# Kernel tuning notes

Measured on AMD Instinct MI355X. Metric: run time of the kernel, lower is better.

The kernel has to match this reference:

```python
import jax, jax.numpy as jnp
import numpy as np

NUM_USERS = 100000
NUM_ITEMS = 50000
NUM_EDGES = 4000000
EMB_DIM = 64
K_HOPS = 3


def setup_inputs() -> dict:
    key = jax.random.key(0)
    k1, k2, k3, k4, k5, k6 = jax.random.split(key, 6)
    N = NUM_USERS + NUM_ITEMS
    return {
        "users_emb": jax.random.normal(k1, (NUM_USERS, EMB_DIM), dtype=jnp.float32) * 0.1,
        "items_emb": jax.random.normal(k2, (NUM_ITEMS, EMB_DIM), dtype=jnp.float32) * 0.1,
        "edge_row": jax.random.randint(k3, (NUM_EDGES,), 0, N, dtype=jnp.int32),
        "edge_col": jax.random.randint(k4, (NUM_EDGES,), 0, N, dtype=jnp.int32),
        "user_id": jax.random.randint(k5, (4096,), 0, NUM_USERS, dtype=jnp.int32),
        "item_ids": jax.random.randint(k6, (4096,), 0, NUM_ITEMS, dtype=jnp.int32),
    }


def reference(users_emb, items_emb, edge_row, edge_col, user_id, item_ids):
    num_users = users_emb.shape[0]
    N = num_users + items_emb.shape[0]
    dt = users_emb.dtype

    # gcn_norm (no self loops): deg = rowsum of A, w_e = d_r^{-1/2} d_c^{-1/2}
    deg = jax.ops.segment_sum(jnp.ones(edge_row.shape[0], dtype=dt), edge_row,
                              num_segments=N)
    deg_inv_sqrt = jnp.where(deg > 0, 1.0 / jnp.sqrt(jnp.where(deg > 0, deg, 1.0)), 0.0)
    w = deg_inv_sqrt[edge_row] * deg_inv_sqrt[edge_col]  # [E]

    emb = jnp.concatenate([users_emb, items_emb], axis=0)  # [N, D]
    acc = emb  # running sum of K+1 layer snapshots
    for _ in range(K_HOPS):
        # SpMM: out[r] += w_e * emb[c]
        emb = jax.ops.segment_sum(w[:, None] * emb[edge_col], edge_row,
                                  num_segments=N)
        acc = acc + emb
    emb_final = acc / (K_HOPS + 1)  # layer-mean pooling

    users_final = emb_final[user_id]               # [B, D]
    items_final = emb_final[num_users + item_ids]  # [B, D]
    return jnp.concatenate([users_final, items_final], axis=1)  # [B, 2D]
```

## Files before the change

kernel.cpp:

```cpp
#include <hip/hip_runtime.h>
#include <hip/hip_bf16.h>

#define NUSERS 100000
#define NITEMS 50000
#define NN (NUSERS + NITEMS)
#define NE 4000000
#define DIM 64
#define BQ 4096
#define NBIN ((NN + 255) >> 8)
#define BINCAP 9216
#define EPB2 8192

typedef unsigned short u16;
typedef unsigned int u32;
typedef float v2f __attribute__((ext_vector_type(2)));

__device__ __forceinline__ float bf2f(u16 u) {
    return __uint_as_float(((unsigned)u) << 16);
}
__device__ __forceinline__ u16 f2bf(float f) {
    unsigned x = __float_as_uint(f);
    return (u16)((x + 0x7FFFu + ((x >> 16) & 1u)) >> 16);
}
__device__ __forceinline__ void add8p(v2f* acc2, uint4 u) {
    acc2[0] += (v2f){__uint_as_float(u.x << 16), __uint_as_float(u.x & 0xffff0000u)};
    acc2[1] += (v2f){__uint_as_float(u.y << 16), __uint_as_float(u.y & 0xffff0000u)};
    acc2[2] += (v2f){__uint_as_float(u.z << 16), __uint_as_float(u.z & 0xffff0000u)};
    acc2[3] += (v2f){__uint_as_float(u.w << 16), __uint_as_float(u.w & 0xffff0000u)};
}
__device__ __forceinline__ uint4 ld_row(const char* __restrict__ base, int c, int dgoff) {
    u32 off = ((u32)c << 7) + (u32)dgoff;
    return *(const uint4*)(base + off);
}

__device__ __forceinline__ void rowsum_core(int start, int n8, int c_all,
                                            const int* __restrict__ col_s,
                                            const char* __restrict__ inb,
                                            int eslot, int dgoff, v2f* acc2) {
    int G = n8 >> 3;
    if (G <= 8) {
        int cg[8];
#pragma unroll
        for (int g = 0; g < 8; ++g)
            cg[g] = __shfl(c_all, (g << 3) + eslot, 64);
        uint4 v[8];
#pragma unroll
        for (int g = 0; g < 8; ++g)
            if (g < G) v[g] = ld_row(inb, cg[g], dgoff);
#pragma unroll
        for (int g = 0; g < 8; ++g)
            if (g < G) add8p(acc2, v[g]);
    } else {
        int i = eslot;
        int c0 = col_s[start + i];
        uint4 v0 = ld_row(inb, c0, dgoff);
        for (i += 8; i < n8; i += 8) {
            int c1 = col_s[start + i];
            uint4 v1 = ld_row(inb, c1, dgoff);
            add8p(acc2, v0);
            v0 = v1;
        }
        add8p(acc2, v0);
    }
}

__device__ __forceinline__ void reduce_acc(v2f* acc2) {
#pragma unroll
    for (int off = 8; off <= 32; off <<= 1)
#pragma unroll
        for (int j = 0; j < 4; ++j) {
            v2f o;
            o.x = __shfl_xor(acc2[j].x, off, 64);
            o.y = __shfl_xor(acc2[j].y, off, 64);
            acc2[j] += o;
        }
}

__global__ void k_init(int* __restrict__ bin_cur, u32* __restrict__ m2w,
                       u16* __restrict__ ea, u16* __restrict__ eb) {
    int t = blockIdx.x * blockDim.x + threadIdx.x;
    if (t < NBIN) bin_cur[t] = t * BINCAP;
    if (t < 37504) m2w[t] = 0;
    if (t < 32) {
        ((u32*)(ea + (size_t)NN * DIM))[t] = 0;
        ((u32*)(eb + (size_t)NN * DIM))[t] = 0;
    }
}

__global__ void __launch_bounds__(1024) k_binA2(
        const int* __restrict__ row, const int* __restrict__ col,
        int* __restrict__ bin_cur, u32* __restrict__ pairs, int E) {
    __shared__ u32 stage[EPB2];
    __shared__ int hist[NBIN];
    __shared__ int base_l[NBIN];
    __shared__ int cbase[NBIN];
    __shared__ int lcur[NBIN];
    __shared__ int s[1024];
    int t = threadIdx.x;
    int base = blockIdx.x * EPB2;
    int lim = min(E - base, EPB2);

    if (t < NBIN) hist[t] = 0;
    __syncthreads();

    for (int i = t; i < lim; i += 1024)
        atomicAdd(&hist[row[base + i] >> 8], 1);
    __syncthreads();

    int v = (t < NBIN) ? hist[t] : 0;
    s[t] = v;
    __syncthreads();
    for (int off = 1; off < 1024; off <<= 1) {
        int x = (t >= off) ? s[t - off] : 0;
        __syncthreads();
        s[t] += x;
        __syncthreads();
    }
    if (t < NBIN) {
        int excl = s[t] - v;
        base_l[t] = excl;
        lcur[t] = excl;
        cbase[t] = (v > 0) ? atomicAdd(&bin_cur[t], v) : 0;
    }
    __syncthreads();

    for (int i = t; i < lim; i += 1024) {
        int r = row[base + i];
        int c = col[base + i];
        int pos = atomicAdd(&lcur[r >> 8], 1);
        stage[pos] = ((u32)(r & 255) << 24) | (u32)c;
    }
    __syncthreads();

    int wv = t >> 6;
    int lane = t & 63;
    for (int b = wv; b < NBIN; b += 16) {
        int h = hist[b];
        int lb = base_l[b];
        size_t gb = (size_t)cbase[b];
        for (int i = lane; i < h; i += 64)
            pairs[gb + i] = stage[lb + i];
    }
}

__global__ void __launch_bounds__(1024) k_binB(
        const u32* __restrict__ pairs, const int* __restrict__ bin_cur,
        int* __restrict__ col_s, int* __restrict__ rs, int* __restrict__ deg) {
    __shared__ int cnt[256];
    __shared__ int pscan[256];
    __shared__ int cur[256];
    int b = blockIdx.x;
    int t = threadIdx.x;
    int base = b * BINCAP;
    int end = bin_cur[b];
    if (t < 256) cnt[t] = 0;
    __syncthreads();
    for (int i = base + t; i < end; i += 1024)
        atomicAdd(&cnt[pairs[i] >> 24], 1);
    __syncthreads();
    int v = (t < 256) ? cnt[t] : 0;
    int pv = (v + 7) & ~7;
    if (t < 256) pscan[t] = pv;
    __syncthreads();
    for (int off = 1; off < 256; off <<= 1) {
        int x = (t >= off && t < 256) ? pscan[t - off] : 0;
        __syncthreads();
        if (t < 256) pscan[t] += x;
        __syncthreads();
    }
    if (t < 256) {
        int rowstart = base + pscan[t] - pv;
        int r = (b << 8) + t;
        if (r < NN) {
            rs[r] = rowstart;
            deg[r] = v;
        }
        cur[t] = rowstart;
        for (int i = v; i < pv; ++i) col_s[rowstart + i] = NN;
    }
    __syncthreads();
    for (int i = base + t; i < end; i += 1024) {
        u32 p = pairs[i];
        int pos = atomicAdd(&cur[p >> 24], 1);
        col_s[pos] = (int)(p & 0x00FFFFFFu);
    }
}

__global__ void k_concat_t0(const float* __restrict__ u, const float* __restrict__ it,
                            const int* __restrict__ deg, u16* __restrict__ emb) {
    int i = blockIdx.x * blockDim.x + threadIdx.x;
    const int NU4 = NUSERS * DIM / 4;
    const int NT4 = NN * DIM / 4;
    if (i >= NT4) return;
    int row = i >> 4;
    int d = deg[row];
    float sc = (d > 0) ? (1.0f / sqrtf((float)d)) : 0.0f;
    float4 v = (i < NU4) ? ((const float4*)u)[i] : ((const float4*)it)[i - NU4];
    ushort4 o;
    o.x = f2bf(sc * v.x); o.y = f2bf(sc * v.y);
    o.z = f2bf(sc * v.z); o.w = f2bf(sc * v.w);
    ((ushort4*)emb)[i] = o;
}

__global__ void k_mark(const int* __restrict__ uid, const int* __restrict__ iid,
                       const int* __restrict__ rs, const int* __restrict__ deg,
                       const int* __restrict__ col_s, unsigned char* __restrict__ m2) {
    int q = (blockIdx.x * blockDim.x + threadIdx.x) >> 6;
    if (q >= 2 * BQ) return;
    int lane = threadIdx.x & 63;
    int r = (q < BQ) ? uid[q] : (NUSERS + iid[q - BQ]);
    if (lane == 0) m2[r] = 1;
    int s = rs[r], n = deg[r];
    for (int i = lane; i < n; i += 64) m2[col_s[s + i]] = 1;
}

__global__ void k_spmm8(const int* __restrict__ rs, const int* __restrict__ deg,
                        const int* __restrict__ col_s, const u16* __restrict__ in,
                        u16* __restrict__ out, const unsigned char* __restrict__ mask) {
    int wid = (blockIdx.x * blockDim.x + threadIdx.x) >> 6;
    if (wid >= NN) return;
    if (mask && !mask[wid]) return;
    int lane = threadIdx.x & 63;
    int eslot = lane >> 3;
    int dg = lane & 7;
    int dgoff = dg << 4;
    int n = deg[wid];
    int start = rs[wid];
    int n8 = (n + 7) & ~7;
    int c_all = col_s[start + lane];
    const char* inb = (const char*)in;
    v2f acc2[4] = {(v2f)0.f, (v2f)0.f, (v2f)0.f, (v2f)0.f};
    if (n8 > 0)
        rowsum_core(start, n8, c_all, col_s, inb, eslot, dgoff, acc2);
    reduce_acc(acc2);
    if (eslot == 0) {
        float s = (n > 0) ? (1.0f / (float)n) : 0.0f;
        v2f vs = {s, s};
        u32 p[4];
#pragma unroll
        for (int j = 0; j < 4; ++j) {
            v2f r = acc2[j] * vs;
            __hip_bfloat162 h = __float22bfloat162_rn(make_float2(r.x, r.y));
            p[j] = *(u32*)&h;
        }
        ((uint4*)out)[(size_t)wid * 8 + dg] = make_uint4(p[0], p[1], p[2], p[3]);
    }
}

__global__ void k_spmm_out(const int* __restrict__ rs, const int* __restrict__ deg,
                           const int* __restrict__ col_s, const u16* __restrict__ in,
                           const int* __restrict__ uid, const int* __restrict__ iid,
                           float* __restrict__ out) {
    int q = (blockIdx.x * blockDim.x + threadIdx.x) >> 6;
    if (q >= 2 * BQ) return;
    int lane = threadIdx.x & 63;
    int eslot = lane >> 3;
    int dg = lane & 7;
    int dgoff = dg << 4;
    int b, r, off;
    if (q < BQ) { b = q; r = uid[q]; off = 0; }
    else { b = q - BQ; r = NUSERS + iid[q - BQ]; off = DIM; }
    int n = deg[r];
    int start = rs[r];
    int n8 = (n + 7) & ~7;
    int c_all = col_s[start + lane];
    const char* inb = (const char*)in;
    v2f acc2[4] = {(v2f)0.f, (v2f)0.f, (v2f)0.f, (v2f)0.f};
    if (n8 > 0)
        rowsum_core(start, n8, c_all, col_s, inb, eslot, dgoff, acc2);
    reduce_acc(acc2);
    if (eslot == 0) {
        float dr = (n > 0) ? (1.0f / sqrtf((float)n)) : 0.0f;
        float* o = out + (size_t)b * (2 * DIM) + off + dg * 8;
#pragma unroll
        for (int j = 0; j < 4; ++j) {
            o[2 * j]     = (o[2 * j]     + dr * acc2[j].x) * 0.25f;
            o[2 * j + 1] = (o[2 * j + 1] + dr * acc2[j].y) * 0.25f;
        }
    }
}


__global__ void k_gather_init(const int* __restrict__ uid, const int* __restrict__ iid,
                              const float* __restrict__ u, const float* __restrict__ it,
                              float* __restrict__ out) {
    int t = blockIdx.x * blockDim.x + threadIdx.x;
    if (t >= BQ * DIM) return;
    int b = t >> 6;
    int d = t & 63;
    out[b * (2 * DIM) + d]       = u[(size_t)uid[b] * DIM + d];
    out[b * (2 * DIM) + DIM + d] = it[(size_t)iid[b] * DIM + d];
}

__global__ void k_gather_add(const int* __restrict__ uid, const int* __restrict__ iid,
                             const int* __restrict__ deg, const u16* __restrict__ emb,
                             float* __restrict__ out) {
    int t = blockIdx.x * blockDim.x + threadIdx.x;
    if (t >= BQ * DIM) return;
    int b = t >> 6;
    int d = t & 63;
    int ru = uid[b];
    int ri = NUSERS + iid[b];
    int du = deg[ru], di = deg[ri];
    float su = (du > 0) ? sqrtf((float)du) : 0.0f;
    float si = (di > 0) ? sqrtf((float)di) : 0.0f;
    int ou = b * (2 * DIM) + d;
    int oi = ou + DIM;
    out[ou] = out[ou] + su * bf2f(emb[(size_t)ru * DIM + d]);
    out[oi] = out[oi] + si * bf2f(emb[(size_t)ri * DIM + d]);
}


extern "C" void kernel_launch(void* const* d_in, const int* in_sizes, int n_in,
                              void* d_out, int out_size, void* d_ws, size_t ws_size,
                              hipStream_t stream) {
    const float* users_emb = (const float*)d_in[0];
    const float* items_emb = (const float*)d_in[1];
    const int*   edge_row  = (const int*)d_in[2];
    const int*   edge_col  = (const int*)d_in[3];
    const int*   user_id   = (const int*)d_in[4];
    const int*   item_ids  = (const int*)d_in[5];
    float* out = (float*)d_out;

    char* ws = (char*)d_ws;
    int*   deg_i   = (int*)  (ws + 0);
    int*   rs      = (int*)  (ws + 655360);
    int*   bin_cur = (int*)  (ws + 1310720);
    unsigned char* m2 = (unsigned char*)(ws + 1400000);
    int*   col_s   = (int*)  (ws + 4194304);
    u32*   pairs   = (u32*)  (ws + 29360128);
    u16*   emb_a   = (u16*)  (ws + 54525952);
    u16*   emb_b   = (u16*)  (ws + 75497472);

    k_init<<<147, 256, 0, stream>>>(bin_cur, (u32*)m2, emb_a, emb_b);

    k_binA2<<<(NE + EPB2 - 1) / EPB2, 1024, 0, stream>>>(edge_row, edge_col, bin_cur,
                                                         pairs, NE);
    k_binB<<<NBIN, 1024, 0, stream>>>(pairs, bin_cur, col_s, rs, deg_i);

    k_concat_t0<<<(NN * DIM / 4 + 255) / 256, 256, 0, stream>>>(users_emb, items_emb,
                                                                deg_i, emb_a);

    k_gather_init<<<(BQ * DIM + 255) / 256, 256, 0, stream>>>(user_id, item_ids,
                                                              users_emb, items_emb, out);

    k_mark<<<(2 * BQ + 3) / 4, 256, 0, stream>>>(user_id, item_ids, rs, deg_i, col_s, m2);

    const int spmm_blocks = (NN + 3) / 4;
    k_spmm8<<<spmm_blocks, 256, 0, stream>>>(rs, deg_i, col_s, emb_a, emb_b,
                                             (const unsigned char*)nullptr);
    k_gather_add<<<(BQ * DIM + 255) / 256, 256, 0, stream>>>(user_id, item_ids, deg_i,
                                                             emb_b, out);
    k_spmm8<<<spmm_blocks, 256, 0, stream>>>(rs, deg_i, col_s, emb_b, emb_a, m2);
    k_gather_add<<<(BQ * DIM + 255) / 256, 256, 0, stream>>>(user_id, item_ids, deg_i,
                                                             emb_a, out);
    k_spmm_out<<<(2 * BQ + 3) / 4, 256, 0, stream>>>(rs, deg_i, col_s, emb_a,
                                                     user_id, item_ids, out);
}
```

Baseline: 307.1 us.

## Fuse embedding scaling into binning, sort columns by range, fold gather_add into output

The binning kernel now sub-buckets each row's columns into coarse column ranges, so the CSR column lists come out roughly sorted and later gathers touch memory more locally. The separate concat/scale kernel is folded into the binning kernel, which removes one launch and one extra pass over the per-row degrees. The last gather_add is dropped and its contribution is added inside the output SpMM by reloading the query row. This costs more shared memory and atomics in k_binB and some extra work per query in the final kernel.

```diff
diff --git a/kernel.cpp b/kernel.cpp
--- a/kernel.cpp
+++ b/kernel.cpp
@@ -10,6 +10,8 @@
 #define NBIN ((NN + 255) >> 8)
 #define BINCAP 9216
 #define EPB2 8192
+#define PSH 14
+#define NP 10
 
 typedef unsigned short u16;
 typedef unsigned int u32;
@@ -145,20 +147,33 @@
 
 __global__ void __launch_bounds__(1024) k_binB(
         const u32* __restrict__ pairs, const int* __restrict__ bin_cur,
-        int* __restrict__ col_s, int* __restrict__ rs, int* __restrict__ deg) {
-    __shared__ int cnt[256];
+        int* __restrict__ col_s, int* __restrict__ rs, int* __restrict__ deg,
+        const float* __restrict__ uemb, const float* __restrict__ itemb,
+        u16* __restrict__ emb) {
+    __shared__ int cnt2[256 * NP];
+    __shared__ int cur2[256 * NP];
     __shared__ int pscan[256];
-    __shared__ int cur[256];
+    __shared__ int degl[256];
     int b = blockIdx.x;
     int t = threadIdx.x;
     int base = b * BINCAP;
     int end = bin_cur[b];
-    if (t < 256) cnt[t] = 0;
-    __syncthreads();
-    for (int i = base + t; i < end; i += 1024)
-        atomicAdd(&cnt[pairs[i] >> 24], 1);
-    __syncthreads();
-    int v = (t < 256) ? cnt[t] : 0;
+    for (int i = t; i < 256 * NP; i += 1024) cnt2[i] = 0;
+    __syncthreads();
+
+    for (int i = base + t; i < end; i += 1024) {
+        u32 p = pairs[i];
+        int row = p >> 24;
+        int c = (int)(p & 0x00FFFFFFu);
+        atomicAdd(&cnt2[row * NP + (c >> PSH)], 1);
+    }
+    __syncthreads();
+
+    int v = 0;
+    if (t < 256) {
+#pragma unroll
+        for (int q = 0; q < NP; ++q) v += cnt2[t * NP + q];
+    }
     int pv = (v + 7) & ~7;
     if (t < 256) pscan[t] = pv;
     __syncthreads();
@@ -170,36 +185,44 @@
     }
     if (t < 256) {
         int rowstart = base + pscan[t] - pv;
+        degl[t] = v;
         int r = (b << 8) + t;
         if (r < NN) {
             rs[r] = rowstart;
             deg[r] = v;
         }
-        cur[t] = rowstart;
+        int acc = rowstart;
+#pragma unroll
+        for (int q = 0; q < NP; ++q) {
+            cur2[t * NP + q] = acc;
+            acc += cnt2[t * NP + q];
+        }
         for (int i = v; i < pv; ++i) col_s[rowstart + i] = NN;
     }
     __syncthreads();
+
     for (int i = base + t; i < end; i += 1024) {
         u32 p = pairs[i];
-        int pos = atomicAdd(&cur[p >> 24], 1);
-        col_s[pos] = (int)(p & 0x00FFFFFFu);
-    }
-}
-
-__global__ void k_concat_t0(const float* __restrict__ u, const float* __restrict__ it,
-                            const int* __restrict__ deg, u16* __restrict__ emb) {
-    int i = blockIdx.x * blockDim.x + threadIdx.x;
-    const int NU4 = NUSERS * DIM / 4;
-    const int NT4 = NN * DIM / 4;
-    if (i >= NT4) return;
-    int row = i >> 4;
-    int d = deg[row];
-    float sc = (d > 0) ? (1.0f / sqrtf((float)d)) : 0.0f;
-    float4 v = (i < NU4) ? ((const float4*)u)[i] : ((const float4*)it)[i - NU4];
-    ushort4 o;
-    o.x = f2bf(sc * v.x); o.y = f2bf(sc * v.y);
-    o.z = f2bf(sc * v.z); o.w = f2bf(sc * v.w);
-    ((ushort4*)emb)[i] = o;
+        int row = p >> 24;
+        int c = (int)(p & 0x00FFFFFFu);
+        int pos = atomicAdd(&cur2[row * NP + (c >> PSH)], 1);
+        col_s[pos] = c;
+    }
+
+    int r0 = b << 8;
+    for (int sIdx = t; sIdx < 256 * 16; sIdx += 1024) {
+        int rl = sIdx >> 4, j = sIdx & 15;
+        int r = r0 + rl;
+        if (r >= NN) continue;
+        int d = degl[rl];
+        float sc = (d > 0) ? (1.0f / sqrtf((float)d)) : 0.0f;
+        float4 vv = (r < NUSERS) ? ((const float4*)uemb)[(size_t)r * 16 + j]
+                                 : ((const float4*)itemb)[(size_t)(r - NUSERS) * 16 + j];
+        ushort4 o;
+        o.x = f2bf(sc * vv.x); o.y = f2bf(sc * vv.y);
+        o.z = f2bf(sc * vv.z); o.w = f2bf(sc * vv.w);
+        ((ushort4*)emb)[(size_t)r * 16 + j] = o;
+    }
 }
 
 __global__ void k_mark(const int* __restrict__ uid, const int* __restrict__ iid,
@@ -271,11 +294,18 @@
     reduce_acc(acc2);
     if (eslot == 0) {
         float dr = (n > 0) ? (1.0f / sqrtf((float)n)) : 0.0f;
+        float sq = (n > 0) ? sqrtf((float)n) : 0.0f;
+        uint4 tv = ld_row(inb, r, dgoff);
+        float tr[8];
+        tr[0] = __uint_as_float(tv.x << 16); tr[1] = __uint_as_float(tv.x & 0xffff0000u);
+        tr[2] = __uint_as_float(tv.y << 16); tr[3] = __uint_as_float(tv.y & 0xffff0000u);
+        tr[4] = __uint_as_float(tv.z << 16); tr[5] = __uint_as_float(tv.z & 0xffff0000u);
+        tr[6] = __uint_as_float(tv.w << 16); tr[7] = __uint_as_float(tv.w & 0xffff0000u);
         float* o = out + (size_t)b * (2 * DIM) + off + dg * 8;
 #pragma unroll
         for (int j = 0; j < 4; ++j) {
-            o[2 * j]     = (o[2 * j]     + dr * acc2[j].x) * 0.25f;
-            o[2 * j + 1] = (o[2 * j + 1] + dr * acc2[j].y) * 0.25f;
+            o[2 * j]     = (o[2 * j]     + sq * tr[2 * j]     + dr * acc2[j].x) * 0.25f;
+            o[2 * j + 1] = (o[2 * j + 1] + sq * tr[2 * j + 1] + dr * acc2[j].y) * 0.25f;
         }
     }
 }
@@ -336,10 +366,8 @@
 
     k_binA2<<<(NE + EPB2 - 1) / EPB2, 1024, 0, stream>>>(edge_row, edge_col, bin_cur,
                                                          pairs, NE);
-    k_binB<<<NBIN, 1024, 0, stream>>>(pairs, bin_cur, col_s, rs, deg_i);
-
-    k_concat_t0<<<(NN * DIM / 4 + 255) / 256, 256, 0, stream>>>(users_emb, items_emb,
-                                                                deg_i, emb_a);
+    k_binB<<<NBIN, 1024, 0, stream>>>(pairs, bin_cur, col_s, rs, deg_i,
+                                      users_emb, items_emb, emb_a);
 
     k_gather_init<<<(BQ * DIM + 255) / 256, 256, 0, stream>>>(user_id, item_ids,
                                                               users_emb, items_emb, out);
@@ -352,8 +380,6 @@
     k_gather_add<<<(BQ * DIM + 255) / 256, 256, 0, stream>>>(user_id, item_ids, deg_i,
                                                              emb_b, out);
     k_spmm8<<<spmm_blocks, 256, 0, stream>>>(rs, deg_i, col_s, emb_b, emb_a, m2);
-    k_gather_add<<<(BQ * DIM + 255) / 256, 256, 0, stream>>>(user_id, item_ids, deg_i,
-                                                             emb_a, out);
     k_spmm_out<<<(2 * BQ + 3) / 4, 256, 0, stream>>>(rs, deg_i, col_s, emb_a,
                                                      user_id, item_ids, out);
 }
```

Measured after the change: 316.2 us. 3.0% more time.
